# Kernel tuning notes

Measured on AMD Instinct MI355X. Metric: run time of the kernel, lower is better.

The kernel has to match this reference:

```python
import jax, jax.numpy as jnp
import numpy as np

B, S, H = 2, 2048, 2048
NH = 16
HD = H // NH  # 128


def setup_inputs() -> dict:
    key = jax.random.key(0)
    ks = jax.random.split(key, 5)
    scale = 1.0 / np.sqrt(H)
    return {
        "hidden_states": jax.random.normal(ks[0], (B, S, H), dtype=jnp.float32),
        "attention_mask": jnp.zeros((B, 1, S, S), dtype=jnp.float32),
        "q_weight": jax.random.normal(ks[1], (H, H), dtype=jnp.float32) * scale,
        "k_weight": jax.random.normal(ks[2], (H, H), dtype=jnp.float32) * scale,
        "v_weight": jax.random.normal(ks[3], (H, H), dtype=jnp.float32) * scale,
        "o_weight": jax.random.normal(ks[4], (H, H), dtype=jnp.float32) * scale,
    }


def reference(hidden_states, attention_mask, q_weight, k_weight, v_weight, o_weight):
    b, s, h = hidden_states.shape
    # Linear(y = x @ W.T), then split heads: [b, nh, s, hd]
    q = (hidden_states @ q_weight.T).reshape(b, s, NH, HD).transpose(0, 2, 1, 3)
    k = (hidden_states @ k_weight.T).reshape(b, s, NH, HD).transpose(0, 2, 1, 3)
    v = (hidden_states @ v_weight.T).reshape(b, s, NH, HD).transpose(0, 2, 1, 3)
    scores = jnp.einsum("bhqd,bhkd->bhqk", q, k) / jnp.sqrt(jnp.float32(HD))
    scores = scores + attention_mask  # additive mask, broadcasts over heads
    attn = jax.nn.softmax(scores, axis=-1)
    out = jnp.einsum("bhqk,bhkd->bhqd", attn, v)
    out = out.transpose(0, 2, 1, 3).reshape(b, s, h)
    return out @ o_weight.T
```

## Files before the change

kernel.cpp:

```cpp
#include <hip/hip_runtime.h>
#include <stdint.h>

constexpr int SEQ   = 2048;
constexpr int NHEAD = 16;
constexpr int HDSZ  = 128;
constexpr int HDIM  = 2048;
constexpr float QK_SCALE = 0.08838834764831845f;

typedef __attribute__((ext_vector_type(8))) __bf16 bf16x8;
typedef __attribute__((ext_vector_type(4))) __bf16 bf16x4;
typedef __attribute__((ext_vector_type(2))) __bf16 bf16x2;
typedef __attribute__((ext_vector_type(4))) float  f32x4;

__device__ __forceinline__ void gl_lds16(const void* gptr, void* lptr) {
  __builtin_amdgcn_global_load_lds(
      (const __attribute__((address_space(1))) unsigned int*)gptr,
      (__attribute__((address_space(3))) unsigned int*)lptr, 16, 0, 0);
}

__global__ __launch_bounds__(256) void cast6_f32_bf16(
    const float* __restrict__ x,  const float* __restrict__ w0,
    const float* __restrict__ w1, const float* __restrict__ w2,
    const float* __restrict__ w3, __bf16* __restrict__ out, int n4) {
  const int y = blockIdx.y;
  const float* src =
      (y == 0) ? x : (y == 1) ? x + (size_t)n4 * 4
      : (y == 2) ? w0 : (y == 3) ? w1 : (y == 4) ? w2 : w3;
  __bf16* dst = out + (size_t)y * (size_t)n4 * 4;
  int i = blockIdx.x * blockDim.x + threadIdx.x;
  int stride = gridDim.x * blockDim.x;
  for (; i < n4; i += stride) {
    float4 v = ((const float4*)src)[i];
    bf16x4 o = { (__bf16)v.x, (__bf16)v.y, (__bf16)v.z, (__bf16)v.w };
    ((bf16x4*)dst)[i] = o;
  }
}

__global__ __launch_bounds__(256) void gemm_qkv(
    const __bf16* __restrict__ A, const __bf16* __restrict__ W,
    __bf16* __restrict__ qkv) {
  constexpr long XN = 4096L * 2048;
  constexpr int K = 2048;
  __shared__ __align__(16) char smem[4 * 16384];
  __bf16* const As0 = (__bf16*)(smem);
  __bf16* const Bs0 = (__bf16*)(smem + 16384);
  __bf16* const As1 = (__bf16*)(smem + 32768);
  __bf16* const Bs1 = (__bf16*)(smem + 49152);
  __bf16* const Ts  = (__bf16*)(smem);

  const int tid  = threadIdx.x;
  const int lane = tid & 63;
  const int w    = tid >> 6;
  const int lg   = lane >> 4, lr = lane & 15;
  const int wr   = w >> 1, wc = w & 1;
  const int flat = blockIdx.y * 48 + blockIdx.x;
  const int x8 = flat & 7, k = flat >> 3;
  const int xm = x8 & 3, xn = x8 >> 2;
  const int mtile = xm * 8 + (k & 7);
  const int ntile = xn * 24 + (k >> 3);
  const long mbase = (long)mtile * 128;
  const long nbase = (long)ntile * 128;

  f32x4 acc[4][4];
#pragma unroll
  for (int i = 0; i < 4; ++i)
#pragma unroll
    for (int j = 0; j < 4; ++j) acc[i][j] = (f32x4){0.f, 0.f, 0.f, 0.f};

  const __bf16* asrc[4];
  const __bf16* wsrc[4];
#pragma unroll
  for (int i = 0; i < 4; ++i) {
    const int row = w * 32 + i * 8 + (lane >> 3);
    const int cs  = ((lane & 7) ^ (row & 7)) * 8;
    asrc[i] = A + (mbase + row) * (long)K + cs;
    wsrc[i] = W + (nbase + row) * (long)K + cs;
  }

  auto stageto = [&](__bf16* As, __bf16* Bs, int ko) {
#pragma unroll
    for (int i = 0; i < 4; ++i) {
      gl_lds16(asrc[i] + ko, &As[(w * 32 + i * 8) * 64]);
      gl_lds16(wsrc[i] + ko, &Bs[(w * 32 + i * 8) * 64]);
    }
  };
  auto computeb = [&](const __bf16* As, const __bf16* Bs) {
#pragma unroll
    for (int kk = 0; kk < 2; ++kk) {
      const int cp = ((kk * 4 + lg) ^ (lr & 7)) << 4;
      bf16x8 af[4], bfv[4];
#pragma unroll
      for (int mm = 0; mm < 4; ++mm)
        af[mm] = *(const bf16x8*)(
            (const char*)As + (wr * 64 + mm * 16 + lr) * 128 + cp);
#pragma unroll
      for (int nn = 0; nn < 4; ++nn)
        bfv[nn] = *(const bf16x8*)(
            (const char*)Bs + (wc * 64 + nn * 16 + lr) * 128 + cp);
      __builtin_amdgcn_s_setprio(1);
#pragma unroll
      for (int nn = 0; nn < 4; ++nn)
#pragma unroll
        for (int mm = 0; mm < 4; ++mm)
          acc[mm][nn] = __builtin_amdgcn_mfma_f32_16x16x32_bf16(
              af[mm], bfv[nn], acc[mm][nn], 0, 0, 0);
      __builtin_amdgcn_s_setprio(0);
    }
  };

  stageto(As0, Bs0, 0);
  __syncthreads();

  int ko = 64;
  for (int tp = 0; tp < 15; ++tp) {
    stageto(As1, Bs1, ko);
    __builtin_amdgcn_sched_barrier(0);
    computeb(As0, Bs0);
    __syncthreads();
    stageto(As0, Bs0, ko + 64);
    __builtin_amdgcn_sched_barrier(0);
    computeb(As1, Bs1);
    __syncthreads();
    ko += 128;
  }
  stageto(As1, Bs1, ko);
  __builtin_amdgcn_sched_barrier(0);
  computeb(As0, Bs0);
  __syncthreads();
  computeb(As1, Bs1);
  __syncthreads();

  const int  mat = ntile >> 4;
  const long nb2 = nbase - (long)mat * 2048;
  const long b   = mbase >> 11, s0 = mbase & 2047;
  const long h   = nb2 >> 7;

  if (mat < 2) {
    __bf16* out = qkv + (size_t)mat * XN;
#pragma unroll
    for (int dh = 0; dh < 2; ++dh) {
      if (wr == dh) {
#pragma unroll
        for (int mm = 0; mm < 4; ++mm)
#pragma unroll
          for (int nn = 0; nn < 4; ++nn) {
            const int d = wc * 64 + nn * 16 + lr;
#pragma unroll
            for (int r = 0; r < 4; ++r)
              Ts[(mm * 16 + lg * 4 + r) * 136 + d] = (__bf16)acc[mm][nn][r];
          }
      }
      __syncthreads();
#pragma unroll
      for (int it = 0; it < 4; ++it) {
        const int idx = it * 256 + tid;
        const int row = idx >> 4, c = idx & 15;
        bf16x8 v = *(const bf16x8*)&Ts[row * 136 + c * 8];
        *(bf16x8*)&out[((b * NHEAD + h) * SEQ + s0 + dh * 64 + row) * HDSZ +
                       c * 8] = v;
      }
      __syncthreads();
    }
  } else {
    __bf16* out = qkv + 2 * XN;
#pragma unroll
    for (int dh = 0; dh < 2; ++dh) {
      if (wc == dh) {
#pragma unroll
        for (int mm = 0; mm < 4; ++mm)
#pragma unroll
          for (int nn = 0; nn < 4; ++nn) {
            const int dd = nn * 16 + lr;
            bf16x4 pk = { (__bf16)acc[mm][nn][0], (__bf16)acc[mm][nn][1],
                          (__bf16)acc[mm][nn][2], (__bf16)acc[mm][nn][3] };
            *(bf16x4*)&Ts[dd * 136 + wr * 64 + mm * 16 + lg * 4] = pk;
          }
      }
      __syncthreads();
#pragma unroll
      for (int it = 0; it < 4; ++it) {
        const int idx = it * 256 + tid;
        const int dd = idx >> 4, c = idx & 15;
        bf16x8 v = *(const bf16x8*)&Ts[dd * 136 + c * 8];
        *(bf16x8*)&out[((b * NHEAD + h) * HDSZ + dh * 64 + dd) * SEQ +
                       s0 + c * 8] = v;
      }
      __syncthreads();
    }
  }
}

__global__ __launch_bounds__(256) void gemm_bt_f32(
    const __bf16* __restrict__ A, const __bf16* __restrict__ B,
    float* __restrict__ C, int M, int N, int K) {
  __shared__ __align__(16) char smem[4 * 16384];
  __bf16* const As0 = (__bf16*)(smem);
  __bf16* const Bs0 = (__bf16*)(smem + 16384);
  __bf16* const As1 = (__bf16*)(smem + 32768);
  __bf16* const Bs1 = (__bf16*)(smem + 49152);

  const int tid  = threadIdx.x;
  const int lane = tid & 63;
  const int w    = tid >> 6;
  const int lg   = lane >> 4, lr = lane & 15;
  const int wr   = w >> 1, wc = w & 1;
  const int flat = blockIdx.y * 16 + blockIdx.x;
  const int x8 = flat & 7, k = flat >> 3;
  const int xm = x8 & 3, xn = x8 >> 2;
  const long mbase = (long)(xm * 8 + (k & 7)) * 128;
  const long nbase = (long)(xn * 8 + (k >> 3)) * 128;

  f32x4 acc[4][4];
#pragma unroll
  for (int i = 0; i < 4; ++i)
#pragma unroll
    for (int j = 0; j < 4; ++j) acc[i][j] = (f32x4){0.f, 0.f, 0.f, 0.f};

  const __bf16* asrc[4];
  const __bf16* bsrc[4];
#pragma unroll
  for (int i = 0; i < 4; ++i) {
    const int row = w * 32 + i * 8 + (lane >> 3);
    const int cs  = ((lane & 7) ^ (row & 7)) * 8;
    asrc[i] = A + (mbase + row) * (long)K + cs;
    bsrc[i] = B + (nbase + row) * (long)K + cs;
  }

  auto stageto = [&](__bf16* As, __bf16* Bs, int ko) {
#pragma unroll
    for (int i = 0; i < 4; ++i) {
      gl_lds16(asrc[i] + ko, &As[(w * 32 + i * 8) * 64]);
      gl_lds16(bsrc[i] + ko, &Bs[(w * 32 + i * 8) * 64]);
    }
  };
  auto computeb = [&](const __bf16* As, const __bf16* Bs) {
#pragma unroll
    for (int kk = 0; kk < 2; ++kk) {
      const int cp = ((kk * 4 + lg) ^ (lr & 7)) << 4;
      bf16x8 af[4], bfv[4];
#pragma unroll
      for (int mm = 0; mm < 4; ++mm)
        af[mm] = *(const bf16x8*)(
            (const char*)As + (wr * 64 + mm * 16 + lr) * 128 + cp);
#pragma unroll
      for (int nn = 0; nn < 4; ++nn)
        bfv[nn] = *(const bf16x8*)(
            (const char*)Bs + (wc * 64 + nn * 16 + lr) * 128 + cp);
      __builtin_amdgcn_s_setprio(1);
#pragma unroll
      for (int nn = 0; nn < 4; ++nn)
#pragma unroll
        for (int mm = 0; mm < 4; ++mm)
          acc[mm][nn] = __builtin_amdgcn_mfma_f32_16x16x32_bf16(
              af[mm], bfv[nn], acc[mm][nn], 0, 0, 0);
      __builtin_amdgcn_s_setprio(0);
    }
  };

  stageto(As0, Bs0, 0);
  __syncthreads();

  int ko = 64;
  for (int tp = 0; tp < 15; ++tp) {
    stageto(As1, Bs1, ko);
    __builtin_amdgcn_sched_barrier(0);
    computeb(As0, Bs0);
    __syncthreads();
    stageto(As0, Bs0, ko + 64);
    __builtin_amdgcn_sched_barrier(0);
    computeb(As1, Bs1);
    __syncthreads();
    ko += 128;
  }
  stageto(As1, Bs1, ko);
  __builtin_amdgcn_sched_barrier(0);
  computeb(As0, Bs0);
  __syncthreads();
  computeb(As1, Bs1);

#pragma unroll
  for (int mm = 0; mm < 4; ++mm)
#pragma unroll
    for (int nn = 0; nn < 4; ++nn) {
      const long n = nbase + wc * 64 + nn * 16 + lr;
#pragma unroll
      for (int r = 0; r < 4; ++r) {
        const long m = mbase + wr * 64 + mm * 16 + lg * 4 + r;
        C[m * (long)N + n] = acc[mm][nn][r];
      }
    }
}

__global__ __launch_bounds__(512, 4) void attn_fused(
    const __bf16* __restrict__ Q, const __bf16* __restrict__ K,
    const __bf16* __restrict__ Vt, const float* __restrict__ mask,
    __bf16* __restrict__ Out) {
  __shared__ __bf16 Ks[2 * 64 * 128];
  __shared__ __bf16 Vs[2 * 128 * 64];
  __shared__ __bf16 Ps[128 * 64];

  const int tid  = threadIdx.x;
  const int lane = tid & 63;
  const int w    = tid >> 6;
  const int lg   = lane >> 4, lr = lane & 15;
  const int flat = blockIdx.y * 16 + blockIdx.x;
  const int swz  = (flat & 7) * 64 + (flat >> 3);
  const int bh   = swz >> 4;
  const int b    = bh >> 4, h = bh & 15;
  const int q0   = (swz & 15) * 128;

  const __bf16* Qh = Q  + (size_t)bh * SEQ * HDSZ;
  const __bf16* Kh = K  + (size_t)bh * SEQ * HDSZ;
  const __bf16* Vh = Vt + (size_t)bh * HDSZ * SEQ;
  const float*  Mb = mask + (size_t)b * SEQ * SEQ;

  bf16x8 qf[4];
#pragma unroll
  for (int kk = 0; kk < 4; ++kk)
    qf[kk] = *(const bf16x8*)(
        Qh + (size_t)(q0 + w * 16 + lr) * HDSZ + kk * 32 + lg * 8);

  const __bf16* ksrc[2];
  const __bf16* vsrc[2];
#pragma unroll
  for (int i = 0; i < 2; ++i) {
    const int ch = i * 512 + tid;
    const int krow = ch >> 4, kc = ch & 15;
    ksrc[i] = Kh + (size_t)krow * HDSZ + (((kc & 8) | ((kc ^ krow) & 7)) * 8);
    const int vrow = ch >> 3, vc = ch & 7;
    vsrc[i] = Vh + (size_t)vrow * SEQ + (((vc ^ vrow) & 7) * 8);
  }

  float mrw = -1e30f, lrw = 0.f;
  f32x4 acco[8];
#pragma unroll
  for (int n = 0; n < 8; ++n) acco[n] = (f32x4){0.f, 0.f, 0.f, 0.f};

#pragma unroll
  for (int i = 0; i < 2; ++i) {
    gl_lds16(ksrc[i], &Ks[(i * 512 + w * 64) * 8]);
    gl_lds16(vsrc[i], &Vs[(i * 512 + w * 64) * 8]);
  }
  __syncthreads();

  constexpr int NT = SEQ / 64;
  for (int t = 0; t < NT; ++t) {
    const int cur = t & 1;
    const int kt = t * 64;
    const char* Kb = (const char*)(Ks + cur * (64 * 128));
    const char* Vb = (const char*)(Vs + cur * (128 * 64));

    f32x4 mk[4];
#pragma unroll
    for (int n = 0; n < 4; ++n)
      mk[n] = *(const f32x4*)(
          Mb + (size_t)(q0 + w * 16 + lr) * SEQ + kt + n * 16 + lg * 4);
    __builtin_amdgcn_sched_barrier(0);

    if (t + 1 < NT) {
      const int nk = kt + 64;
      __bf16* Kn = Ks + (cur ^ 1) * (64 * 128);
      __bf16* Vn = Vs + (cur ^ 1) * (128 * 64);
#pragma unroll
      for (int i = 0; i < 2; ++i) {
        gl_lds16(ksrc[i] + (size_t)nk * HDSZ, &Kn[(i * 512 + w * 64) * 8]);
        gl_lds16(vsrc[i] + nk, &Vn[(i * 512 + w * 64) * 8]);
      }
    }
    __builtin_amdgcn_sched_barrier(0);

    f32x4 sacc[4];
#pragma unroll
    for (int n = 0; n < 4; ++n) sacc[n] = (f32x4){0.f, 0.f, 0.f, 0.f};
    __builtin_amdgcn_s_setprio(1);
#pragma unroll
    for (int n = 0; n < 4; ++n)
#pragma unroll
      for (int kk = 0; kk < 4; ++kk) {
        const int cp = (kk * 4 + lg) ^ (lr & 7);
        bf16x8 kf = *(const bf16x8*)(Kb + ((n * 16 + lr) << 8) + (cp << 4));
        sacc[n] = __builtin_amdgcn_mfma_f32_16x16x32_bf16(kf, qf[kk], sacc[n], 0, 0, 0);
      }
    __builtin_amdgcn_s_setprio(0);

    float sv[4][4];
    float tm = -1e30f;
#pragma unroll
    for (int n = 0; n < 4; ++n)
#pragma unroll
      for (int r = 0; r < 4; ++r) {
        float x = fmaf(sacc[n][r], QK_SCALE, mk[n][r]);
        sv[n][r] = x;
        tm = fmaxf(tm, x);
      }
    tm = fmaxf(tm, __shfl_xor(tm, 16));
    tm = fmaxf(tm, __shfl_xor(tm, 32));
    const float mn = fmaxf(mrw, tm);
    const float corr = __expf(mrw - mn);
    mrw = mn;
    float ls = 0.f;
#pragma unroll
    for (int n = 0; n < 4; ++n)
#pragma unroll
      for (int r = 0; r < 4; ++r) {
        float p = __expf(sv[n][r] - mn);
        sv[n][r] = p;
        ls += p;
      }
    ls += __shfl_xor(ls, 16);
    ls += __shfl_xor(ls, 32);
    lrw = lrw * corr + ls;
    float cb[4];
#pragma unroll
    for (int r = 0; r < 4; ++r) cb[r] = __shfl(corr, lg * 4 + r);
#pragma unroll
    for (int n = 0; n < 8; ++n)
#pragma unroll
      for (int r = 0; r < 4; ++r) acco[n][r] *= cb[r];

#pragma unroll
    for (int n = 0; n < 4; ++n)
#pragma unroll
      for (int rp = 0; rp < 2; ++rp) {
        bf16x2 pk = { (__bf16)sv[n][2 * rp], (__bf16)sv[n][2 * rp + 1] };
        const int pbyte = (n * 32 + lg * 8 + rp * 4) ^ ((lr & 7) << 4);
        *(bf16x2*)((char*)Ps + (w * 16 + lr) * 128 + pbyte) = pk;
      }
    __asm__ volatile("s_waitcnt lgkmcnt(0)" ::: "memory");
    __builtin_amdgcn_sched_barrier(0);

    __builtin_amdgcn_s_setprio(1);
#pragma unroll
    for (int kk = 0; kk < 2; ++kk) {
      const int pcp = (kk * 4 + lg) ^ (lr & 7);
      bf16x8 pa = *(const bf16x8*)(
          (const char*)Ps + (w * 16 + lr) * 128 + (pcp << 4));
#pragma unroll
      for (int n = 0; n < 8; ++n) {
        const int cp = (kk * 4 + lg) ^ (lr & 7);
        bf16x8 vf = *(const bf16x8*)(Vb + ((n * 16 + lr) << 7) + (cp << 4));
        acco[n] = __builtin_amdgcn_mfma_f32_16x16x32_bf16(pa, vf, acco[n], 0, 0, 0);
      }
    }
    __builtin_amdgcn_s_setprio(0);

    __syncthreads();
  }

  float lb[4];
#pragma unroll
  for (int r = 0; r < 4; ++r) lb[r] = __shfl(lrw, lg * 4 + r);
#pragma unroll
  for (int r = 0; r < 4; ++r) {
    const float inv = 1.0f / lb[r];
    const int srow = q0 + w * 16 + lg * 4 + r;
    const size_t base = ((size_t)b * SEQ + srow) * HDIM + h * HDSZ;
#pragma unroll
    for (int n = 0; n < 8; ++n)
      Out[base + n * 16 + lr] = (__bf16)(acco[n][r] * inv);
  }
}

extern "C" void kernel_launch(void* const* d_in, const int* in_sizes, int n_in,
                              void* d_out, int out_size, void* d_ws, size_t ws_size,
                              hipStream_t stream) {
  const float* x    = (const float*)d_in[0];
  const float* mask = (const float*)d_in[1];
  const float* wq   = (const float*)d_in[2];
  const float* wk   = (const float*)d_in[3];
  const float* wv   = (const float*)d_in[4];
  const float* wo   = (const float*)d_in[5];

  constexpr long XN = 4096L * 2048;
  constexpr long WN = 2048L * 2048;

  __bf16* xbf = (__bf16*)d_ws;
  __bf16* wqb = xbf + XN;
  __bf16* wob = wqb + 3 * WN;
  __bf16* qw  = wqb + 4 * WN;
  __bf16* kw  = qw + XN;
  __bf16* vtw = kw + XN;
  __bf16* aw  = vtw + XN;

  cast6_f32_bf16<<<dim3(256, 6), 256, 0, stream>>>(x, wq, wk, wv, wo, xbf,
                                                   (int)(WN / 4));

  gemm_qkv<<<dim3(48, 32), 256, 0, stream>>>(xbf, wqb, qw);

  attn_fused<<<dim3(16, 32), 512, 0, stream>>>(qw, kw, vtw, mask, aw);

  gemm_bt_f32<<<dim3(16, 32), 256, 0, stream>>>(aw, wob, (float*)d_out,
                                                4096, 2048, 2048);
}
```

Before: 279.5 us.

## Use 32x32x16 MFMA in attention and pass P through registers instead of LDS

Reworks the fused attention kernel to use 4 waves, each owning 32 query rows, with 32x32x16 bf16 MFMA for both QK^T and PV in place of 16x16x32 MFMA. The softmax probabilities are packed to bf16 and swapped between half-waves with cross-lane shuffles to form the PV A operand, which removes the Ps LDS buffer, its writes and the lgkmcnt wait. Larger MFMA tiles reduce LDS fragment reads per flop. The cost is higher register pressure (launch bounds drop to 256 threads, 2 blocks) and fewer waves per block for hiding latency.

Measured after the change: 339.3 us. +21.4%, slower.

```diff
diff --git a/kernel.cpp b/kernel.cpp
--- a/kernel.cpp
+++ b/kernel.cpp
@@ -7,15 +7,22 @@
 constexpr int HDIM  = 2048;
 constexpr float QK_SCALE = 0.08838834764831845f;
 
-typedef __attribute__((ext_vector_type(8))) __bf16 bf16x8;
-typedef __attribute__((ext_vector_type(4))) __bf16 bf16x4;
-typedef __attribute__((ext_vector_type(2))) __bf16 bf16x2;
-typedef __attribute__((ext_vector_type(4))) float  f32x4;
+typedef __attribute__((ext_vector_type(8)))  __bf16 bf16x8;
+typedef __attribute__((ext_vector_type(4)))  __bf16 bf16x4;
+typedef __attribute__((ext_vector_type(2)))  __bf16 bf16x2;
+typedef __attribute__((ext_vector_type(4)))  float  f32x4;
+typedef __attribute__((ext_vector_type(16))) float  f32x16;
+typedef __attribute__((ext_vector_type(4)))  unsigned int uint4v;
 
 __device__ __forceinline__ void gl_lds16(const void* gptr, void* lptr) {
   __builtin_amdgcn_global_load_lds(
       (const __attribute__((address_space(1))) unsigned int*)gptr,
       (__attribute__((address_space(3))) unsigned int*)lptr, 16, 0, 0);
+}
+
+__device__ __forceinline__ unsigned int pk2(float a, float b) {
+  bf16x2 t = { (__bf16)a, (__bf16)b };
+  return __builtin_bit_cast(unsigned int, t);
 }
 
 __global__ __launch_bounds__(256) void cast6_f32_bf16(
@@ -291,18 +298,18 @@
     }
 }
 
-__global__ __launch_bounds__(512, 4) void attn_fused(
+__global__ __launch_bounds__(256, 2) void attn_fused(
     const __bf16* __restrict__ Q, const __bf16* __restrict__ K,
     const __bf16* __restrict__ Vt, const float* __restrict__ mask,
     __bf16* __restrict__ Out) {
   __shared__ __bf16 Ks[2 * 64 * 128];
   __shared__ __bf16 Vs[2 * 128 * 64];
-  __shared__ __bf16 Ps[128 * 64];
 
   const int tid  = threadIdx.x;
   const int lane = tid & 63;
   const int w    = tid >> 6;
-  const int lg   = lane >> 4, lr = lane & 15;
+  const int hi   = lane >> 5;
+  const int l5   = lane & 31;
   const int flat = blockIdx.y * 16 + blockIdx.x;
   const int swz  = (flat & 7) * 64 + (flat >> 3);
   const int bh   = swz >> 4;
@@ -314,17 +321,17 @@
   const __bf16* Vh = Vt + (size_t)bh * HDSZ * SEQ;
   const float*  Mb = mask + (size_t)b * SEQ * SEQ;
 
-  bf16x8 qf[4];
-#pragma unroll
-  for (int kk = 0; kk < 4; ++kk)
-    qf[kk] = *(const bf16x8*)(
-        Qh + (size_t)(q0 + w * 16 + lr) * HDSZ + kk * 32 + lg * 8);
-
-  const __bf16* ksrc[2];
-  const __bf16* vsrc[2];
-#pragma unroll
-  for (int i = 0; i < 2; ++i) {
-    const int ch = i * 512 + tid;
+  const int qrow = q0 + w * 32 + l5;
+  bf16x8 qf[8];
+#pragma unroll
+  for (int ds = 0; ds < 8; ++ds)
+    qf[ds] = *(const bf16x8*)(Qh + (size_t)qrow * HDSZ + ds * 16 + hi * 8);
+
+  const __bf16* ksrc[4];
+  const __bf16* vsrc[4];
+#pragma unroll
+  for (int i = 0; i < 4; ++i) {
+    const int ch = i * 256 + tid;
     const int krow = ch >> 4, kc = ch & 15;
     ksrc[i] = Kh + (size_t)krow * HDSZ + (((kc & 8) | ((kc ^ krow) & 7)) * 8);
     const int vrow = ch >> 3, vc = ch & 7;
@@ -332,14 +339,16 @@
   }
 
   float mrw = -1e30f, lrw = 0.f;
-  f32x4 acco[8];
-#pragma unroll
-  for (int n = 0; n < 8; ++n) acco[n] = (f32x4){0.f, 0.f, 0.f, 0.f};
-
-#pragma unroll
-  for (int i = 0; i < 2; ++i) {
-    gl_lds16(ksrc[i], &Ks[(i * 512 + w * 64) * 8]);
-    gl_lds16(vsrc[i], &Vs[(i * 512 + w * 64) * 8]);
+  f32x16 acco[4];
+#pragma unroll
+  for (int dt = 0; dt < 4; ++dt)
+#pragma unroll
+    for (int r = 0; r < 16; ++r) acco[dt][r] = 0.f;
+
+#pragma unroll
+  for (int i = 0; i < 4; ++i) {
+    gl_lds16(ksrc[i], &Ks[(i * 256 + w * 64) * 8]);
+    gl_lds16(vsrc[i], &Vs[(i * 256 + w * 64) * 8]);
   }
   __syncthreads();
 
@@ -350,11 +359,13 @@
     const char* Kb = (const char*)(Ks + cur * (64 * 128));
     const char* Vb = (const char*)(Vs + cur * (128 * 64));
 
-    f32x4 mk[4];
-#pragma unroll
-    for (int n = 0; n < 4; ++n)
-      mk[n] = *(const f32x4*)(
-          Mb + (size_t)(q0 + w * 16 + lr) * SEQ + kt + n * 16 + lg * 4);
+    f32x4 mk[2][4];
+#pragma unroll
+    for (int n = 0; n < 2; ++n)
+#pragma unroll
+      for (int g = 0; g < 4; ++g)
+        mk[n][g] = *(const f32x4*)(
+            Mb + (size_t)qrow * SEQ + kt + n * 32 + 8 * g + 4 * hi);
     __builtin_amdgcn_sched_barrier(0);
 
     if (t + 1 < NT) {
@@ -362,84 +373,98 @@
       __bf16* Kn = Ks + (cur ^ 1) * (64 * 128);
       __bf16* Vn = Vs + (cur ^ 1) * (128 * 64);
 #pragma unroll
-      for (int i = 0; i < 2; ++i) {
-        gl_lds16(ksrc[i] + (size_t)nk * HDSZ, &Kn[(i * 512 + w * 64) * 8]);
-        gl_lds16(vsrc[i] + nk, &Vn[(i * 512 + w * 64) * 8]);
+      for (int i = 0; i < 4; ++i) {
+        gl_lds16(ksrc[i] + (size_t)nk * HDSZ, &Kn[(i * 256 + w * 64) * 8]);
+        gl_lds16(vsrc[i] + nk, &Vn[(i * 256 + w * 64) * 8]);
       }
     }
     __builtin_amdgcn_sched_barrier(0);
 
-    f32x4 sacc[4];
-#pragma unroll
-    for (int n = 0; n < 4; ++n) sacc[n] = (f32x4){0.f, 0.f, 0.f, 0.f};
+    f32x16 sacc[2];
+#pragma unroll
+    for (int n = 0; n < 2; ++n)
+#pragma unroll
+      for (int r = 0; r < 16; ++r) sacc[n][r] = 0.f;
     __builtin_amdgcn_s_setprio(1);
 #pragma unroll
-    for (int n = 0; n < 4; ++n)
-#pragma unroll
-      for (int kk = 0; kk < 4; ++kk) {
-        const int cp = (kk * 4 + lg) ^ (lr & 7);
-        bf16x8 kf = *(const bf16x8*)(Kb + ((n * 16 + lr) << 8) + (cp << 4));
-        sacc[n] = __builtin_amdgcn_mfma_f32_16x16x32_bf16(kf, qf[kk], sacc[n], 0, 0, 0);
-      }
+    for (int n = 0; n < 2; ++n) {
+      const int kr = n * 32 + l5;
+#pragma unroll
+      for (int ds = 0; ds < 8; ++ds) {
+        const int g = 2 * ds + hi;
+        bf16x8 kf = *(const bf16x8*)(
+            Kb + kr * 256 + (((g & 8) | ((g ^ kr) & 7)) << 4));
+        sacc[n] = __builtin_amdgcn_mfma_f32_32x32x16_bf16(kf, qf[ds],
+                                                          sacc[n], 0, 0, 0);
+      }
+    }
     __builtin_amdgcn_s_setprio(0);
 
-    float sv[4][4];
+    float x[2][16];
     float tm = -1e30f;
 #pragma unroll
-    for (int n = 0; n < 4; ++n)
-#pragma unroll
-      for (int r = 0; r < 4; ++r) {
-        float x = fmaf(sacc[n][r], QK_SCALE, mk[n][r]);
-        sv[n][r] = x;
-        tm = fmaxf(tm, x);
-      }
-    tm = fmaxf(tm, __shfl_xor(tm, 16));
+    for (int n = 0; n < 2; ++n)
+#pragma unroll
+      for (int r = 0; r < 16; ++r) {
+        float v = fmaf(sacc[n][r], QK_SCALE, mk[n][r >> 2][r & 3]);
+        x[n][r] = v;
+        tm = fmaxf(tm, v);
+      }
     tm = fmaxf(tm, __shfl_xor(tm, 32));
     const float mn = fmaxf(mrw, tm);
     const float corr = __expf(mrw - mn);
     mrw = mn;
     float ls = 0.f;
-#pragma unroll
-    for (int n = 0; n < 4; ++n)
-#pragma unroll
-      for (int r = 0; r < 4; ++r) {
-        float p = __expf(sv[n][r] - mn);
-        sv[n][r] = p;
-        ls += p;
-      }
-    ls += __shfl_xor(ls, 16);
+    unsigned int pr[2][4][2];
+#pragma unroll
+    for (int n = 0; n < 2; ++n)
+#pragma unroll
+      for (int g = 0; g < 4; ++g)
+#pragma unroll
+        for (int j = 0; j < 2; ++j) {
+          float p0 = __expf(x[n][4 * g + 2 * j]     - mn);
+          float p1 = __expf(x[n][4 * g + 2 * j + 1] - mn);
+          ls += p0 + p1;
+          pr[n][g][j] = pk2(p0, p1);
+        }
     ls += __shfl_xor(ls, 32);
     lrw = lrw * corr + ls;
-    float cb[4];
-#pragma unroll
-    for (int r = 0; r < 4; ++r) cb[r] = __shfl(corr, lg * 4 + r);
-#pragma unroll
-    for (int n = 0; n < 8; ++n)
-#pragma unroll
-      for (int r = 0; r < 4; ++r) acco[n][r] *= cb[r];
-
-#pragma unroll
-    for (int n = 0; n < 4; ++n)
-#pragma unroll
-      for (int rp = 0; rp < 2; ++rp) {
-        bf16x2 pk = { (__bf16)sv[n][2 * rp], (__bf16)sv[n][2 * rp + 1] };
-        const int pbyte = (n * 32 + lg * 8 + rp * 4) ^ ((lr & 7) << 4);
-        *(bf16x2*)((char*)Ps + (w * 16 + lr) * 128 + pbyte) = pk;
-      }
-    __asm__ volatile("s_waitcnt lgkmcnt(0)" ::: "memory");
-    __builtin_amdgcn_sched_barrier(0);
+
+    float cb[16];
+#pragma unroll
+    for (int r = 0; r < 16; ++r)
+      cb[r] = __shfl(corr, (r & 3) + 8 * (r >> 2) + 4 * hi);
+#pragma unroll
+    for (int dt = 0; dt < 4; ++dt)
+#pragma unroll
+      for (int r = 0; r < 16; ++r) acco[dt][r] *= cb[r];
+
+    bf16x8 pa[4];
+#pragma unroll
+    for (int ks = 0; ks < 4; ++ks) {
+      const int n = ks >> 1, ge = (ks & 1) * 2;
+      unsigned int s0 = hi ? pr[n][ge][0] : pr[n][ge + 1][0];
+      unsigned int s1 = hi ? pr[n][ge][1] : pr[n][ge + 1][1];
+      unsigned int r0 = __shfl_xor((int)s0, 32);
+      unsigned int r1 = __shfl_xor((int)s1, 32);
+      unsigned int o0 = pr[n][ge + hi][0];
+      unsigned int o1 = pr[n][ge + hi][1];
+      uint4v pw = { hi ? r0 : o0, hi ? r1 : o1,
+                    hi ? o0 : r0, hi ? o1 : r1 };
+      pa[ks] = __builtin_bit_cast(bf16x8, pw);
+    }
 
     __builtin_amdgcn_s_setprio(1);
 #pragma unroll
-    for (int kk = 0; kk < 2; ++kk) {
-      const int pcp = (kk * 4 + lg) ^ (lr & 7);
-      bf16x8 pa = *(const bf16x8*)(
-          (const char*)Ps + (w * 16 + lr) * 128 + (pcp << 4));
-#pragma unroll
-      for (int n = 0; n < 8; ++n) {
-        const int cp = (kk * 4 + lg) ^ (lr & 7);
-        bf16x8 vf = *(const bf16x8*)(Vb + ((n * 16 + lr) << 7) + (cp << 4));
-        acco[n] = __builtin_amdgcn_mfma_f32_16x16x32_bf16(pa, vf, acco[n], 0, 0, 0);
+    for (int ks = 0; ks < 4; ++ks) {
+      const int g = 2 * ks + hi;
+#pragma unroll
+      for (int dt = 0; dt < 4; ++dt) {
+        const int vd = dt * 32 + l5;
+        bf16x8 vf = *(const bf16x8*)(
+            Vb + vd * 128 + (((g ^ vd) & 7) << 4));
+        acco[dt] = __builtin_amdgcn_mfma_f32_32x32x16_bf16(pa[ks], vf,
+                                                           acco[dt], 0, 0, 0);
       }
     }
     __builtin_amdgcn_s_setprio(0);
@@ -447,18 +472,18 @@
     __syncthreads();
   }
 
-  float lb[4];
-#pragma unroll
-  for (int r = 0; r < 4; ++r) lb[r] = __shfl(lrw, lg * 4 + r);
-#pragma unroll
-  for (int r = 0; r < 4; ++r) {
-    const float inv = 1.0f / lb[r];
-    const int srow = q0 + w * 16 + lg * 4 + r;
-    const size_t base = ((size_t)b * SEQ + srow) * HDIM + h * HDSZ;
-#pragma unroll
-    for (int n = 0; n < 8; ++n)
-      Out[base + n * 16 + lr] = (__bf16)(acco[n][r] * inv);
-  }
+  float inv[16];
+#pragma unroll
+  for (int r = 0; r < 16; ++r)
+    inv[r] = 1.0f / __shfl(lrw, (r & 3) + 8 * (r >> 2) + 4 * hi);
+#pragma unroll
+  for (int dt = 0; dt < 4; ++dt)
+#pragma unroll
+    for (int r = 0; r < 16; ++r) {
+      const int q = q0 + w * 32 + (r & 3) + 8 * (r >> 2) + 4 * hi;
+      Out[((size_t)b * SEQ + q) * HDIM + h * HDSZ + dt * 32 + l5] =
+          (__bf16)(acco[dt][r] * inv[r]);
+    }
 }
 
 extern "C" void kernel_launch(void* const* d_in, const int* in_sizes, int n_in,
@@ -487,7 +512,7 @@
 
   gemm_qkv<<<dim3(48, 32), 256, 0, stream>>>(xbf, wqb, qw);
 
-  attn_fused<<<dim3(16, 32), 512, 0, stream>>>(qw, kw, vtw, mask, aw);
+  attn_fused<<<dim3(16, 32), 256, 0, stream>>>(qw, kw, vtw, mask, aw);
 
   gemm_bt_f32<<<dim3(16, 32), 256, 0, stream>>>(aw, wob, (float*)d_out,
                                                 4096, 2048, 2048);
```

## Split attention KV tiles across wave pairs with 32-row Q per wave and lazy rescale

Applied to the files above, without the earlier changes.

Each wave now owns 32 query rows (two 16-row tiles) and half of each 64-key tile. Each K fragment read from LDS feeds two MFMAs, and each V fragment is reused across both row tiles. The two wave halves keep separate online-softmax states, which are merged through shared memory at the end. The accumulator rescale is skipped unless the running max grows by more than 8, which saves exp and multiply work per tile. The cost is more accumulator registers (two sets of 8 f32x4), a larger LDS footprint of 80KB that may limit occupancy, and an extra merge step.

New measurement: 631.5 us. 2.26x slower.

```diff
diff --git a/kernel.cpp b/kernel.cpp
--- a/kernel.cpp
+++ b/kernel.cpp
@@ -295,14 +295,17 @@
     const __bf16* __restrict__ Q, const __bf16* __restrict__ K,
     const __bf16* __restrict__ Vt, const float* __restrict__ mask,
     __bf16* __restrict__ Out) {
-  __shared__ __bf16 Ks[2 * 64 * 128];
-  __shared__ __bf16 Vs[2 * 128 * 64];
-  __shared__ __bf16 Ps[128 * 64];
+  __shared__ __align__(16) char sm[81920];
+  __bf16* const Ks = (__bf16*)sm;
+  __bf16* const Vs = (__bf16*)(sm + 32768);
+  char*   const Pb = sm + 65536;
 
   const int tid  = threadIdx.x;
   const int lane = tid & 63;
   const int w    = tid >> 6;
   const int lg   = lane >> 4, lr = lane & 15;
+  const int qw   = w & 3;
+  const int kh   = w >> 2;
   const int flat = blockIdx.y * 16 + blockIdx.x;
   const int swz  = (flat & 7) * 64 + (flat >> 3);
   const int bh   = swz >> 4;
@@ -314,11 +317,14 @@
   const __bf16* Vh = Vt + (size_t)bh * HDSZ * SEQ;
   const float*  Mb = mask + (size_t)b * SEQ * SEQ;
 
-  bf16x8 qf[4];
-#pragma unroll
-  for (int kk = 0; kk < 4; ++kk)
-    qf[kk] = *(const bf16x8*)(
-        Qh + (size_t)(q0 + w * 16 + lr) * HDSZ + kk * 32 + lg * 8);
+  const int qb = q0 + qw * 32;
+  bf16x8 qf[2][4];
+#pragma unroll
+  for (int rt = 0; rt < 2; ++rt)
+#pragma unroll
+    for (int kk = 0; kk < 4; ++kk)
+      qf[rt][kk] = *(const bf16x8*)(
+          Qh + (size_t)(qb + rt * 16 + lr) * HDSZ + kk * 32 + lg * 8);
 
   const __bf16* ksrc[2];
   const __bf16* vsrc[2];
@@ -331,10 +337,12 @@
     vsrc[i] = Vh + (size_t)vrow * SEQ + (((vc ^ vrow) & 7) * 8);
   }
 
-  float mrw = -1e30f, lrw = 0.f;
-  f32x4 acco[8];
-#pragma unroll
-  for (int n = 0; n < 8; ++n) acco[n] = (f32x4){0.f, 0.f, 0.f, 0.f};
+  float mrw[2] = {-1e30f, -1e30f}, lrw[2] = {0.f, 0.f};
+  f32x4 acco[2][8];
+#pragma unroll
+  for (int rt = 0; rt < 2; ++rt)
+#pragma unroll
+    for (int n = 0; n < 8; ++n) acco[rt][n] = (f32x4){0.f, 0.f, 0.f, 0.f};
 
 #pragma unroll
   for (int i = 0; i < 2; ++i) {
@@ -342,6 +350,8 @@
     gl_lds16(vsrc[i], &Vs[(i * 512 + w * 64) * 8]);
   }
   __syncthreads();
+
+  char* const Pw = Pb + w * 2048;
 
   constexpr int NT = SEQ / 64;
   for (int t = 0; t < NT; ++t) {
@@ -350,11 +360,14 @@
     const char* Kb = (const char*)(Ks + cur * (64 * 128));
     const char* Vb = (const char*)(Vs + cur * (128 * 64));
 
-    f32x4 mk[4];
-#pragma unroll
-    for (int n = 0; n < 4; ++n)
-      mk[n] = *(const f32x4*)(
-          Mb + (size_t)(q0 + w * 16 + lr) * SEQ + kt + n * 16 + lg * 4);
+    f32x4 mk[2][2];
+#pragma unroll
+    for (int rt = 0; rt < 2; ++rt)
+#pragma unroll
+      for (int n = 0; n < 2; ++n)
+        mk[rt][n] = *(const f32x4*)(
+            Mb + (size_t)(qb + rt * 16 + lr) * SEQ + kt + kh * 32 +
+            n * 16 + lg * 4);
     __builtin_amdgcn_sched_barrier(0);
 
     if (t + 1 < NT) {
@@ -369,95 +382,135 @@
     }
     __builtin_amdgcn_sched_barrier(0);
 
-    f32x4 sacc[4];
-#pragma unroll
-    for (int n = 0; n < 4; ++n) sacc[n] = (f32x4){0.f, 0.f, 0.f, 0.f};
+    f32x4 sacc[2][2];
+#pragma unroll
+    for (int rt = 0; rt < 2; ++rt)
+#pragma unroll
+      for (int n = 0; n < 2; ++n) sacc[rt][n] = (f32x4){0.f, 0.f, 0.f, 0.f};
     __builtin_amdgcn_s_setprio(1);
 #pragma unroll
-    for (int n = 0; n < 4; ++n)
+    for (int n = 0; n < 2; ++n) {
+      const int kr = kh * 32 + n * 16 + lr;
 #pragma unroll
       for (int kk = 0; kk < 4; ++kk) {
         const int cp = (kk * 4 + lg) ^ (lr & 7);
-        bf16x8 kf = *(const bf16x8*)(Kb + ((n * 16 + lr) << 8) + (cp << 4));
-        sacc[n] = __builtin_amdgcn_mfma_f32_16x16x32_bf16(kf, qf[kk], sacc[n], 0, 0, 0);
-      }
+        bf16x8 kf = *(const bf16x8*)(Kb + (kr << 8) + (cp << 4));
+        sacc[0][n] = __builtin_amdgcn_mfma_f32_16x16x32_bf16(kf, qf[0][kk], sacc[0][n], 0, 0, 0);
+        sacc[1][n] = __builtin_amdgcn_mfma_f32_16x16x32_bf16(kf, qf[1][kk], sacc[1][n], 0, 0, 0);
+      }
+    }
     __builtin_amdgcn_s_setprio(0);
 
-    float sv[4][4];
-    float tm = -1e30f;
-#pragma unroll
-    for (int n = 0; n < 4; ++n)
+#pragma unroll
+    for (int rt = 0; rt < 2; ++rt) {
+      float sv[2][4];
+      float tm = -1e30f;
+#pragma unroll
+      for (int n = 0; n < 2; ++n)
+#pragma unroll
+        for (int r = 0; r < 4; ++r) {
+          float x = fmaf(sacc[rt][n][r], QK_SCALE, mk[rt][n][r]);
+          sv[n][r] = x;
+          tm = fmaxf(tm, x);
+        }
+      tm = fmaxf(tm, __shfl_xor(tm, 16));
+      tm = fmaxf(tm, __shfl_xor(tm, 32));
+      if (!__all(tm <= mrw[rt] + 8.f)) {
+        const float mn = fmaxf(mrw[rt], tm);
+        const float corr = __expf(mrw[rt] - mn);
+        mrw[rt] = mn;
+        lrw[rt] *= corr;
+        float cb[4];
+#pragma unroll
+        for (int r = 0; r < 4; ++r) cb[r] = __shfl(corr, lg * 4 + r);
+#pragma unroll
+        for (int n = 0; n < 8; ++n)
+#pragma unroll
+          for (int r = 0; r < 4; ++r) acco[rt][n][r] *= cb[r];
+      }
+      float ls = 0.f;
+#pragma unroll
+      for (int n = 0; n < 2; ++n)
+#pragma unroll
+        for (int r = 0; r < 4; ++r) {
+          float p = __expf(sv[n][r] - mrw[rt]);
+          sv[n][r] = p;
+          ls += p;
+        }
+      ls += __shfl_xor(ls, 16);
+      ls += __shfl_xor(ls, 32);
+      lrw[rt] += ls;
+#pragma unroll
+      for (int n = 0; n < 2; ++n)
+#pragma unroll
+        for (int rp = 0; rp < 2; ++rp) {
+          bf16x2 pk = { (__bf16)sv[n][2 * rp], (__bf16)sv[n][2 * rp + 1] };
+          const int pbyte = (n * 32 + lg * 8 + rp * 4) ^ ((lr & 3) << 4);
+          *(bf16x2*)(Pw + (rt * 16 + lr) * 64 + pbyte) = pk;
+        }
+    }
+    __asm__ volatile("s_waitcnt lgkmcnt(0)" ::: "memory");
+    __builtin_amdgcn_sched_barrier(0);
+
+    __builtin_amdgcn_s_setprio(1);
+    bf16x8 pa0 = *(const bf16x8*)(
+        Pw + (lr) * 64 + ((lg ^ (lr & 3)) << 4));
+    bf16x8 pa1 = *(const bf16x8*)(
+        Pw + (16 + lr) * 64 + ((lg ^ (lr & 3)) << 4));
+#pragma unroll
+    for (int n = 0; n < 8; ++n) {
+      const int vd = n * 16 + lr;
+      const int cp = (kh * 4 + lg) ^ (lr & 7);
+      bf16x8 vf = *(const bf16x8*)(Vb + (vd << 7) + (cp << 4));
+      acco[0][n] = __builtin_amdgcn_mfma_f32_16x16x32_bf16(pa0, vf, acco[0][n], 0, 0, 0);
+      acco[1][n] = __builtin_amdgcn_mfma_f32_16x16x32_bf16(pa1, vf, acco[1][n], 0, 0, 0);
+    }
+    __builtin_amdgcn_s_setprio(0);
+
+    __syncthreads();
+  }
+
+  f32x4* const fb  = (f32x4*)sm;
+  float* const mlm = (float*)(sm + 65536);
+  float* const mll = mlm + 512;
+  if (kh == 1) {
+#pragma unroll
+    for (int rt = 0; rt < 2; ++rt) {
+#pragma unroll
+      for (int n = 0; n < 8; ++n)
+        fb[(rt * 8 + n) * 256 + qw * 64 + lane] = acco[rt][n];
+      mlm[(qw * 2 + rt) * 64 + lane] = mrw[rt];
+      mll[(qw * 2 + rt) * 64 + lane] = lrw[rt];
+    }
+  }
+  __syncthreads();
+  if (kh == 0) {
+#pragma unroll
+    for (int rt = 0; rt < 2; ++rt) {
+      const float m1 = mlm[(qw * 2 + rt) * 64 + lane];
+      const float l1 = mll[(qw * 2 + rt) * 64 + lane];
+      const float M  = fmaxf(mrw[rt], m1);
+      const float a0 = __expf(mrw[rt] - M);
+      const float a1 = __expf(m1 - M);
+      const float lc = lrw[rt] * a0 + l1 * a1;
+      float a0r[4], a1r[4], invr[4];
 #pragma unroll
       for (int r = 0; r < 4; ++r) {
-        float x = fmaf(sacc[n][r], QK_SCALE, mk[n][r]);
-        sv[n][r] = x;
-        tm = fmaxf(tm, x);
-      }
-    tm = fmaxf(tm, __shfl_xor(tm, 16));
-    tm = fmaxf(tm, __shfl_xor(tm, 32));
-    const float mn = fmaxf(mrw, tm);
-    const float corr = __expf(mrw - mn);
-    mrw = mn;
-    float ls = 0.f;
-#pragma unroll
-    for (int n = 0; n < 4; ++n)
-#pragma unroll
-      for (int r = 0; r < 4; ++r) {
-        float p = __expf(sv[n][r] - mn);
-        sv[n][r] = p;
-        ls += p;
-      }
-    ls += __shfl_xor(ls, 16);
-    ls += __shfl_xor(ls, 32);
-    lrw = lrw * corr + ls;
-    float cb[4];
-#pragma unroll
-    for (int r = 0; r < 4; ++r) cb[r] = __shfl(corr, lg * 4 + r);
-#pragma unroll
-    for (int n = 0; n < 8; ++n)
-#pragma unroll
-      for (int r = 0; r < 4; ++r) acco[n][r] *= cb[r];
-
-#pragma unroll
-    for (int n = 0; n < 4; ++n)
-#pragma unroll
-      for (int rp = 0; rp < 2; ++rp) {
-        bf16x2 pk = { (__bf16)sv[n][2 * rp], (__bf16)sv[n][2 * rp + 1] };
-        const int pbyte = (n * 32 + lg * 8 + rp * 4) ^ ((lr & 7) << 4);
-        *(bf16x2*)((char*)Ps + (w * 16 + lr) * 128 + pbyte) = pk;
-      }
-    __asm__ volatile("s_waitcnt lgkmcnt(0)" ::: "memory");
-    __builtin_amdgcn_sched_barrier(0);
-
-    __builtin_amdgcn_s_setprio(1);
-#pragma unroll
-    for (int kk = 0; kk < 2; ++kk) {
-      const int pcp = (kk * 4 + lg) ^ (lr & 7);
-      bf16x8 pa = *(const bf16x8*)(
-          (const char*)Ps + (w * 16 + lr) * 128 + (pcp << 4));
+        a0r[r] = __shfl(a0, lg * 4 + r);
+        a1r[r] = __shfl(a1, lg * 4 + r);
+        invr[r] = 1.0f / __shfl(lc, lg * 4 + r);
+      }
 #pragma unroll
       for (int n = 0; n < 8; ++n) {
-        const int cp = (kk * 4 + lg) ^ (lr & 7);
-        bf16x8 vf = *(const bf16x8*)(Vb + ((n * 16 + lr) << 7) + (cp << 4));
-        acco[n] = __builtin_amdgcn_mfma_f32_16x16x32_bf16(pa, vf, acco[n], 0, 0, 0);
-      }
-    }
-    __builtin_amdgcn_s_setprio(0);
-
-    __syncthreads();
-  }
-
-  float lb[4];
-#pragma unroll
-  for (int r = 0; r < 4; ++r) lb[r] = __shfl(lrw, lg * 4 + r);
-#pragma unroll
-  for (int r = 0; r < 4; ++r) {
-    const float inv = 1.0f / lb[r];
-    const int srow = q0 + w * 16 + lg * 4 + r;
-    const size_t base = ((size_t)b * SEQ + srow) * HDIM + h * HDSZ;
-#pragma unroll
-    for (int n = 0; n < 8; ++n)
-      Out[base + n * 16 + lr] = (__bf16)(acco[n][r] * inv);
+        f32x4 pn = fb[(rt * 8 + n) * 256 + qw * 64 + lane];
+#pragma unroll
+        for (int r = 0; r < 4; ++r) {
+          const int srow = qb + rt * 16 + lg * 4 + r;
+          Out[((size_t)b * SEQ + srow) * HDIM + h * HDSZ + n * 16 + lr] =
+              (__bf16)((acco[rt][n][r] * a0r[r] + pn[r] * a1r[r]) * invr[r]);
+        }
+      }
+    }
   }
 }
 
```
